# Kernel optimization log

Hardware: AMD Instinct MI355X
Metric: run time of the kernel (lower is better)

Reference implementation:

```python
import jax, jax.numpy as jnp
import numpy as np

B, S, T = 512, 1024, 48

def setup_inputs() -> dict:
    key = jax.random.key(0)
    k1, k2, k3, k4, k5 = jax.random.split(key, 5)
    emissions = jax.random.normal(k1, (B, S, T), dtype=jnp.float32)
    tags = jax.random.randint(k2, (B, S), 0, T, dtype=jnp.int32)
    mask = jnp.ones((B, S), dtype=jnp.float32)
    transitions = jax.random.normal(k3, (T, T), dtype=jnp.float32)
    start_transitions = jax.random.normal(k4, (T,), dtype=jnp.float32)
    end_transitions = jax.random.normal(k5, (T,), dtype=jnp.float32)
    return {"emissions": emissions, "tags": tags, "mask": mask,
            "transitions": transitions, "start_transitions": start_transitions,
            "end_transitions": end_transitions}

def _crf_loss(emissions, transitions, start_transitions, end_transitions, tags, mask):
    # ---- numerator: score of the gold path (fully vectorized over seq) ----
    emit = jnp.take_along_axis(emissions, tags[..., None], axis=2)[..., 0]  # (B,S)
    trans = transitions[tags[:, 1:], tags[:, :-1]]                          # (B,S-1)
    lengths = jnp.sum(mask, axis=1).astype(jnp.int32)
    last_idx = jnp.clip(lengths - 1, 0)
    last_tags = jnp.take_along_axis(tags, last_idx[:, None], axis=1)[:, 0]
    numerator = (start_transitions[tags[:, 0]] + emit[:, 0]
                 + jnp.sum(mask[:, 1:] * (emit[:, 1:] + trans), axis=1)
                 + end_transitions[last_tags])                               # (B,)

    # ---- denominator: log-partition via forward algorithm (lax.scan) ----
    def step(score, x):
        em_i, m_i = x  # (B,T), (B,)
        # logsumexp over previous tag; emission is prev-independent so add outside
        nxt = jax.nn.logsumexp(score[:, :, None] + transitions.T[None, :, :], axis=1) + em_i
        score = jnp.where(m_i[:, None] > 0, nxt, score)
        return score, None

    init = start_transitions[None, :] + emissions[:, 0]                      # (B,T)
    xs = (jnp.swapaxes(emissions[:, 1:], 0, 1), jnp.swapaxes(mask[:, 1:], 0, 1))
    final, _ = jax.lax.scan(step, init, xs)
    denominator = jax.nn.logsumexp(final + end_transitions[None, :], axis=1)  # (B,)

    return jnp.mean(denominator - numerator)

def reference(emissions, tags, mask, transitions, start_transitions, end_transitions):
    return _crf_loss(emissions, transitions, start_transitions, end_transitions, tags, mask)
```

## Files before the change

kernel.cpp:

```cpp
#include <hip/hip_runtime.h>
#include <math.h>

#define Bn 512
#define Sn 1024
#define Tn 48
#define NSEG 16
#define SEGLEN 64

typedef _Float16 h2 __attribute__((ext_vector_type(2)));
typedef _Float16 h4 __attribute__((ext_vector_type(4)));
typedef float    f4 __attribute__((ext_vector_type(4)));

static constexpr float LOG2E = 1.4426950408889634f;
static constexpr float LN2f  = 0.6931471805599453f;

#define MFMA16(A, B, C) __builtin_amdgcn_mfma_f32_16x16x16f16((A), (B), (C), 0, 0, 0)

__device__ __forceinline__ h2 hmax2(h2 a, h2 b) {
#if __has_builtin(__builtin_elementwise_max)
  return __builtin_elementwise_max(a, b);
#else
  h2 r;
  r[0] = a[0] > b[0] ? a[0] : b[0];
  r[1] = a[1] > b[1] ? a[1] : b[1];
  return r;
#endif
}
__device__ __forceinline__ h2 cvt2(float a, float b) {
  return __builtin_bit_cast(h2, __builtin_amdgcn_cvt_pkrtz(a, b));
}
__device__ __forceinline__ h4 mkh4(h2 lo, h2 hi) {
  return __builtin_shufflevector(lo, hi, 0, 1, 2, 3);
}
__device__ __forceinline__ h2 loh(h4 v) { return __builtin_shufflevector(v, v, 0, 1); }
__device__ __forceinline__ h2 hih(h4 v) { return __builtin_shufflevector(v, v, 2, 3); }

__global__ __launch_bounds__(256) void ehgen(const float* __restrict__ em,
                                             _Float16* __restrict__ out) {
  const size_t total = (size_t)Bn * Sn * Tn;
  const size_t i = ((size_t)blockIdx.x * 256 + threadIdx.x) * 8;
  if (i >= total) return;
  const f4 a = *(const f4*)(em + i);
  const f4 b = *(const f4*)(em + i + 4);
  h4 o1, o2;
  #pragma unroll
  for (int j = 0; j < 4; ++j) {
    o1[j] = (_Float16)__builtin_amdgcn_exp2f(fmaf(a[j], LOG2E, -6.0f));
    o2[j] = (_Float16)__builtin_amdgcn_exp2f(fmaf(b[j], LOG2E, -6.0f));
  }
  *(h4*)(out + i) = o1;
  *(h4*)(out + i + 4) = o2;
}

template <bool PRE>
__global__ __launch_bounds__(1024, 2)
void crf_fwd_seg(const float* __restrict__ em,
                 const float* __restrict__ mask,
                 const float* __restrict__ trans,
                 const float* __restrict__ startt,
                 const float* __restrict__ endt,
                 const _Float16* __restrict__ eh16,
                 float* __restrict__ den_out)
{
  const int b   = blockIdx.x;
  const int tid = threadIdx.x;
  const int wid = tid >> 6;
  const int l   = tid & 63;
  const int c16 = l & 15;
  const int g   = l >> 4;

  __shared__ __align__(16) _Float16 Lm16[NSEG][48][50];
  __shared__ float Loff[NSEG][48];
  __shared__ float lwbuf[64];

  const float*    __restrict__ emb = em + (size_t)b * Sn * Tn;
  const float*    __restrict__ mkb = mask + (size_t)b * Sn;
  const _Float16* __restrict__ ehL = PRE ? (eh16 + (size_t)b * Sn * Tn + 4 * g) : nullptr;
  const float*    __restrict__ emL = emb + 4 * g;

  h4 Afr[3][3];
  float mtg;
  {
    float tl[3][3][4];
    float mt = -1e30f;
    #pragma unroll
    for (int rt = 0; rt < 3; ++rt)
      #pragma unroll
      for (int kt = 0; kt < 3; ++kt) {
        const f4 t4 = *(const f4*)(trans + (16 * rt + c16) * Tn + 16 * kt + 4 * g);
        #pragma unroll
        for (int i = 0; i < 4; ++i) {
          const float v = t4[i] * LOG2E;
          tl[rt][kt][i] = v;
          mt = fmaxf(mt, v);
        }
      }
    #pragma unroll
    for (int off = 1; off < 64; off <<= 1) mt = fmaxf(mt, __shfl_xor(mt, off));
    mtg = mt;
    #pragma unroll
    for (int rt = 0; rt < 3; ++rt)
      #pragma unroll
      for (int kt = 0; kt < 3; ++kt) {
        h4 r;
        #pragma unroll
        for (int i = 0; i < 4; ++i)
          r[i] = (_Float16)__builtin_amdgcn_exp2f(tl[rt][kt][i] - mtg);
        Afr[rt][kt] = r;
      }
  }

  h4 Bfr[3][3];
  float Mc[3] = {0.f, 0.f, 0.f};
  float cnt = 0.f;
  #pragma unroll
  for (int kt = 0; kt < 3; ++kt)
    #pragma unroll
    for (int ct = 0; ct < 3; ++ct) {
      h4 r;
      #pragma unroll
      for (int i = 0; i < 4; ++i)
        r[i] = (_Float16)(((16 * kt + 4 * g + i) == (16 * ct + c16)) ? 1.0f : 0.0f);
      Bfr[kt][ct] = r;
    }

  auto STEP = [&](const h4& e0, const h4& e1, const h4& e2, float mkval,
                  bool APPLY, const float (&scv)[3], const float (&shv)[3]) {
    if (__int_as_float(__builtin_amdgcn_readfirstlane(__float_as_int(mkval))) > 0.0f) {
      f4 acc[3][3];
      #pragma unroll
      for (int rt = 0; rt < 3; ++rt)
        #pragma unroll
        for (int ct = 0; ct < 3; ++ct) acc[rt][ct] = f4{0.f, 0.f, 0.f, 0.f};
      #pragma unroll
      for (int kt = 0; kt < 3; ++kt)
        #pragma unroll
        for (int rt = 0; rt < 3; ++rt)
          #pragma unroll
          for (int ct = 0; ct < 3; ++ct)
            acc[rt][ct] = MFMA16(Afr[rt][kt], Bfr[kt][ct], acc[rt][ct]);
      const h4 ehv[3] = {e0, e1, e2};
      #pragma unroll
      for (int rt = 0; rt < 3; ++rt) {
        const h2 elo = loh(ehv[rt]);
        const h2 ehi = hih(ehv[rt]);
        #pragma unroll
        for (int ct = 0; ct < 3; ++ct) {
          f4 a = acc[rt][ct];
          if (APPLY) {
            a[0] *= scv[ct]; a[1] *= scv[ct]; a[2] *= scv[ct]; a[3] *= scv[ct];
          }
          const h2 lo = cvt2(a[0], a[1]) * elo;
          const h2 hi = cvt2(a[2], a[3]) * ehi;
          Bfr[rt][ct] = mkh4(lo, hi);
        }
      }
      if (APPLY) { Mc[0] += shv[0]; Mc[1] += shv[1]; Mc[2] += shv[2]; }
      cnt += 1.0f;
    }
  };

  auto MEASURE = [&](float (&sh)[3], float (&sc)[3]) {
    #pragma unroll
    for (int ct = 0; ct < 3; ++ct) {
      h2 m = loh(Bfr[0][ct]);
      m = hmax2(m, hih(Bfr[0][ct]));
      m = hmax2(m, loh(Bfr[1][ct]));
      m = hmax2(m, hih(Bfr[1][ct]));
      m = hmax2(m, loh(Bfr[2][ct]));
      m = hmax2(m, hih(Bfr[2][ct]));
      m = hmax2(m, __builtin_bit_cast(h2, __shfl_xor(__builtin_bit_cast(int, m), 16)));
      m = hmax2(m, __builtin_bit_cast(h2, __shfl_xor(__builtin_bit_cast(int, m), 32)));
      const float mf = fmaxf((float)m[0], (float)m[1]);
      int eb = ((__float_as_int(mf) >> 23) & 0xff) - 127;
      eb = eb < -15 ? -15 : (eb > 15 ? 15 : eb);
      sh[ct] = (float)eb;
      sc[ct] = __int_as_float((127 - eb) << 23);
    }
  };

  auto loadEH = [&](int s, h4& x, h4& y, h4& z) {
    if constexpr (PRE) {
      const _Float16* p = ehL + (size_t)s * Tn;
      x = *(const h4*)(p);
      y = *(const h4*)(p + 16);
      z = *(const h4*)(p + 32);
    } else {
      const float* p = emL + (size_t)s * Tn;
      const f4 a = *(const f4*)(p);
      const f4 b2 = *(const f4*)(p + 16);
      const f4 c2 = *(const f4*)(p + 32);
      f4 ea, eb2, ec;
      #pragma unroll
      for (int i = 0; i < 4; ++i) {
        ea[i]  = __builtin_amdgcn_exp2f(fmaf(a[i],  LOG2E, -6.0f));
        eb2[i] = __builtin_amdgcn_exp2f(fmaf(b2[i], LOG2E, -6.0f));
        ec[i]  = __builtin_amdgcn_exp2f(fmaf(c2[i], LOG2E, -6.0f));
      }
      x = mkh4(cvt2(ea[0], ea[1]), cvt2(ea[2], ea[3]));
      y = mkh4(cvt2(eb2[0], eb2[1]), cvt2(eb2[2], eb2[3]));
      z = mkh4(cvt2(ec[0], ec[1]), cvt2(ec[2], ec[3]));
    }
  };

  const int s_begin = 1 + SEGLEN * wid;
  const int nchunk  = (wid == NSEG - 1) ? 15 : 16;
  float shP[3] = {0.f, 0.f, 0.f}, scP[3] = {1.f, 1.f, 1.f};
  float shA[3] = {0.f, 0.f, 0.f}, scA[3] = {1.f, 1.f, 1.f};
  const float sh1[3] = {0.f, 0.f, 0.f};
  const float sc1[3] = {1.f, 1.f, 1.f};

  h4 E0, E1, E2, N0, N1, N2;
  f4 mkc = *(const f4*)(mkb + s_begin);
  f4 mkn;
  loadEH(s_begin, E0, E1, E2);
  int s = s_begin;
  #pragma unroll 1
  for (int c = 0; c < nchunk; ++c) {
    mkn = *(const f4*)(mkb + ((c + 1 < nchunk) ? (s + 4) : s));
    loadEH(s + 1, N0, N1, N2);
    STEP(E0, E1, E2, mkc[0], false, sc1, sh1);
    loadEH(s + 2, E0, E1, E2);
    STEP(N0, N1, N2, mkc[1], true, scP, shP);
    MEASURE(shA, scA);
    loadEH(s + 3, N0, N1, N2);
    STEP(E0, E1, E2, mkc[2], false, sc1, sh1);
    loadEH(s + 4, E0, E1, E2);
    STEP(N0, N1, N2, mkc[3], true, scA, shA);
    MEASURE(shP, scP);
    mkc = mkn;
    s += 4;
  }
  if (wid == NSEG - 1) {
    loadEH(1022, N0, N1, N2);
    STEP(E0, E1, E2, mkb[1021], false, sc1, sh1);
    loadEH(1023, E0, E1, E2);
    STEP(N0, N1, N2, mkb[1022], true, scP, shP);
    MEASURE(shA, scA);
    STEP(E0, E1, E2, mkb[1023], false, sc1, sh1);
  }

  const float addc = (mtg + 6.0f) * cnt;
  #pragma unroll
  for (int kt = 0; kt < 3; ++kt)
    #pragma unroll
    for (int ct = 0; ct < 3; ++ct)
      #pragma unroll
      for (int i = 0; i < 4; ++i)
        Lm16[wid][16 * kt + 4 * g + i][16 * ct + c16] =
            (_Float16)__builtin_amdgcn_logf((float)Bfr[kt][ct][i]);
  if (g == 0) {
    #pragma unroll
    for (int ct = 0; ct < 3; ++ct) Loff[wid][16 * ct + c16] = Mc[ct] + addc;
  }
  __syncthreads();

  if (wid == 0) {
    float lw = -INFINITY;
    if (l < Tn) lw = (startt[l] + emb[l]) * LOG2E;
    #pragma unroll 1
    for (int sg = 0; sg < NSEG; ++sg) {
      lwbuf[l] = (l < Tn) ? (lw + Loff[sg][l]) : -INFINITY;
      float nlw = lw;
      if (l < Tn) {
        float mj = -INFINITY;
        for (int cc = 0; cc < Tn; ++cc)
          mj = fmaxf(mj, (float)Lm16[sg][l][cc] + lwbuf[cc]);
        float ssum = 0.f;
        for (int cc = 0; cc < Tn; ++cc)
          ssum += __builtin_amdgcn_exp2f((float)Lm16[sg][l][cc] + lwbuf[cc] - mj);
        nlw = mj + __builtin_amdgcn_logf(ssum);
      }
      lw = nlw;
    }
    float v = (l < Tn) ? lw + endt[l] * LOG2E : -INFINITY;
    float mv = v;
    #pragma unroll
    for (int off = 32; off; off >>= 1) mv = fmaxf(mv, __shfl_xor(mv, off));
    float zz = (l < Tn) ? __builtin_amdgcn_exp2f(v - mv) : 0.f;
    #pragma unroll
    for (int off = 32; off; off >>= 1) zz += __shfl_xor(zz, off);
    if (l == 0) den_out[b] = (mv + __builtin_amdgcn_logf(zz)) * LN2f;
  }
}

__global__ __launch_bounds__(256) void crf_numer(
    const float* __restrict__ em, const int* __restrict__ tags,
    const float* __restrict__ mask, const float* __restrict__ trans,
    const float* __restrict__ startt, const float* __restrict__ endt,
    float* __restrict__ num_out)
{
  const int b = blockIdx.x, t = threadIdx.x;
  const int*   tgb = tags + (size_t)b * Sn;
  const float* mkb = mask + (size_t)b * Sn;
  const float* emb = em + (size_t)b * Sn * Tn;

  const int s0 = t * 4;
  const int4 tg = *(const int4*)(tgb + s0);
  const f4   mk = *(const f4*)(mkb + s0);
  const int  tprev = (t == 0) ? 0 : tgb[s0 - 1];
  const int  tgarr[5] = {tprev, tg.x, tg.y, tg.z, tg.w};

  float acc  = 0.0f;
  float msum = mk[0] + mk[1] + mk[2] + mk[3];
  #pragma unroll
  for (int i = 0; i < 4; ++i) {
    const int s = s0 + i;
    if (s >= 1)
      acc += mk[i] * (emb[(size_t)s * Tn + tgarr[i + 1]] +
                      trans[tgarr[i + 1] * Tn + tgarr[i]]);
  }
  #pragma unroll
  for (int off = 32; off; off >>= 1) {
    acc  += __shfl_xor(acc, off);
    msum += __shfl_xor(msum, off);
  }
  __shared__ float ra[4], rm[4];
  if ((t & 63) == 0) { ra[t >> 6] = acc; rm[t >> 6] = msum; }
  __syncthreads();
  if (t == 0) {
    const float a = ra[0] + ra[1] + ra[2] + ra[3];
    const float m = rm[0] + rm[1] + rm[2] + rm[3];
    int last = (int)(m + 0.5f) - 1;
    if (last < 0) last = 0;
    const int lt = tgb[last];
    const int t0 = tgb[0];
    num_out[b] = startt[t0] + emb[t0] + a + endt[lt];
  }
}

__global__ __launch_bounds__(512) void reduce_loss(const float* __restrict__ den,
                                                   const float* __restrict__ num,
                                                   float* __restrict__ out) {
  __shared__ float red[8];
  const int t = threadIdx.x;
  float v = den[t] - num[t];
  #pragma unroll
  for (int off = 32; off; off >>= 1) v += __shfl_xor(v, off);
  if ((t & 63) == 0) red[t >> 6] = v;
  __syncthreads();
  if (t == 0) {
    float s = 0.f;
    #pragma unroll
    for (int wv = 0; wv < 8; ++wv) s += red[wv];
    out[0] = s * (1.0f / 512.0f);
  }
}

extern "C" void kernel_launch(void* const* d_in, const int* in_sizes, int n_in,
                              void* d_out, int out_size, void* d_ws, size_t ws_size,
                              hipStream_t stream) {
  const float* emissions = (const float*)d_in[0];
  const int*   tags      = (const int*)d_in[1];
  const float* mask      = (const float*)d_in[2];
  const float* trans     = (const float*)d_in[3];
  const float* startt    = (const float*)d_in[4];
  const float* endt      = (const float*)d_in[5];
  float* den_ws = (float*)d_ws;
  float* num_ws = den_ws + Bn;
  const size_t ehoff   = 4096;
  const size_t ehbytes = (size_t)Bn * Sn * Tn * sizeof(_Float16);
  _Float16* eh16 = (_Float16*)((char*)d_ws + ehoff);
  const bool pre = (ws_size >= ehoff + ehbytes);

  crf_numer<<<Bn, 256, 0, stream>>>(emissions, tags, mask, trans, startt, endt, num_ws);
  if (pre) {
    const int total8 = Bn * Sn * Tn / 8;
    ehgen<<<(total8 + 255) / 256, 256, 0, stream>>>(emissions, eh16);
    crf_fwd_seg<true><<<Bn, 1024, 0, stream>>>(emissions, mask, trans, startt, endt,
                                               eh16, den_ws);
  } else {
    crf_fwd_seg<false><<<Bn, 1024, 0, stream>>>(emissions, mask, trans, startt, endt,
                                                nullptr, den_ws);
  }
  reduce_loss<<<1, 512, 0, stream>>>(den_ws, num_ws, (float*)d_out);
}
```

Measured before the change: 227.8 us.

## Chain segment transfer matrices in-register instead of via log-domain LDS matrices

Each segment's wave now applies its own linear-domain transfer matrix to the running score vector, using a max-shifted exp, FMA and cross-lane shuffle reductions, passing the result through a small LDS buffer with a barrier per segment. This replaces converting every matrix to fp16 log values in LDS and having wave 0 run a serial 48x48 logsumexp per segment. It removes the large LDS arrays and the per-element exp/log work, at the cost of 16 block-wide barriers. The precision model changes because fp16 linear-domain matrix entries are used directly rather than their logs.

```diff
diff --git a/kernel.cpp b/kernel.cpp
--- a/kernel.cpp
+++ b/kernel.cpp
@@ -69,8 +69,6 @@
   const int c16 = l & 15;
   const int g   = l >> 4;
 
-  __shared__ __align__(16) _Float16 Lm16[NSEG][48][50];
-  __shared__ float Loff[NSEG][48];
   __shared__ float lwbuf[64];
 
   const float*    __restrict__ emb = em + (size_t)b * Sn * Tn;
@@ -241,39 +239,45 @@
   }
 
   const float addc = (mtg + 6.0f) * cnt;
-  #pragma unroll
-  for (int kt = 0; kt < 3; ++kt)
-    #pragma unroll
-    for (int ct = 0; ct < 3; ++ct)
-      #pragma unroll
-      for (int i = 0; i < 4; ++i)
-        Lm16[wid][16 * kt + 4 * g + i][16 * ct + c16] =
-            (_Float16)__builtin_amdgcn_logf((float)Bfr[kt][ct][i]);
-  if (g == 0) {
-    #pragma unroll
-    for (int ct = 0; ct < 3; ++ct) Loff[wid][16 * ct + c16] = Mc[ct] + addc;
-  }
+  if (wid == 0 && l < Tn) lwbuf[l] = (startt[l] + emb[l]) * LOG2E;
   __syncthreads();
+  #pragma unroll 1
+  for (int sg = 0; sg < NSEG; ++sg) {
+    if (wid == sg) {
+      const float u0 = lwbuf[c16]      + Mc[0] + addc;
+      const float u1 = lwbuf[16 + c16] + Mc[1] + addc;
+      const float u2 = lwbuf[32 + c16] + Mc[2] + addc;
+      float um = fmaxf(u0, fmaxf(u1, u2));
+      #pragma unroll
+      for (int off = 1; off < 64; off <<= 1) um = fmaxf(um, __shfl_xor(um, off));
+      const float p0 = __builtin_amdgcn_exp2f(u0 - um);
+      const float p1 = __builtin_amdgcn_exp2f(u1 - um);
+      const float p2 = __builtin_amdgcn_exp2f(u2 - um);
+      float rs[3][4];
+      #pragma unroll
+      for (int kt = 0; kt < 3; ++kt)
+        #pragma unroll
+        for (int i = 0; i < 4; ++i) {
+          float v = (float)Bfr[kt][0][i] * p0;
+          v = fmaf((float)Bfr[kt][1][i], p1, v);
+          v = fmaf((float)Bfr[kt][2][i], p2, v);
+          #pragma unroll
+          for (int off = 1; off < 16; off <<= 1) v += __shfl_xor(v, off);
+          rs[kt][i] = v;
+        }
+      if (c16 == 0) {
+        #pragma unroll
+        for (int kt = 0; kt < 3; ++kt)
+          #pragma unroll
+          for (int i = 0; i < 4; ++i)
+            lwbuf[16 * kt + 4 * g + i] = um + __builtin_amdgcn_logf(rs[kt][i]);
+      }
+    }
+    __syncthreads();
+  }
 
   if (wid == 0) {
-    float lw = -INFINITY;
-    if (l < Tn) lw = (startt[l] + emb[l]) * LOG2E;
-    #pragma unroll 1
-    for (int sg = 0; sg < NSEG; ++sg) {
-      lwbuf[l] = (l < Tn) ? (lw + Loff[sg][l]) : -INFINITY;
-      float nlw = lw;
-      if (l < Tn) {
-        float mj = -INFINITY;
-        for (int cc = 0; cc < Tn; ++cc)
-          mj = fmaxf(mj, (float)Lm16[sg][l][cc] + lwbuf[cc]);
-        float ssum = 0.f;
-        for (int cc = 0; cc < Tn; ++cc)
-          ssum += __builtin_amdgcn_exp2f((float)Lm16[sg][l][cc] + lwbuf[cc] - mj);
-        nlw = mj + __builtin_amdgcn_logf(ssum);
-      }
-      lw = nlw;
-    }
-    float v = (l < Tn) ? lw + endt[l] * LOG2E : -INFINITY;
+    float v = (l < Tn) ? lwbuf[l] + endt[l] * LOG2E : -INFINITY;
     float mv = v;
     #pragma unroll
     for (int off = 32; off; off >>= 1) mv = fmaxf(mv, __shfl_xor(mv, off));
```

Result: no change. 227.6 us (-0.1%).
